# Optimization experiments

Measured on AMD Instinct MI355X. Metric: run time of the kernel, lower is better.

The kernel has to match this reference:

```python
import math
import jax, jax.numpy as jnp
import numpy as np

B, T, D_MODEL, H, D = 2, 1024, 1024, 16, 64
NUM_LEVELS = int(math.ceil(math.log2(T + 1))) + 1  # 12 for max_seq_len=1024


def _fenwick_level(idx):
    return (idx & -idx).bit_length() - 1


def build_fenwick_masks(T, num_levels):
    """NumPy replica of the torch build_fenwick_masks; returns [L, T, T] float32."""
    j_to_nodes = {}
    for j in range(1, T + 1):
        nodes = []
        idx = j
        while idx <= T:
            nodes.append((idx, _fenwick_level(idx)))
            idx += idx & -idx
        j_to_nodes[j] = nodes
    t_to_query_nodes = {}
    for t in range(1, T + 1):
        s = set()
        idx = t
        while idx > 0:
            s.add(idx)
            idx -= idx & -idx
        t_to_query_nodes[t] = s
    masks = np.zeros((num_levels, T, T), dtype=np.float32)
    for t in range(1, T + 1):
        qn = t_to_query_nodes[t]
        for j in range(1, t + 1):
            for node_idx, node_level in j_to_nodes[j]:
                if node_idx in qn:
                    masks[min(node_level, num_levels - 1), t - 1, j - 1] = 1.0
                    break
    return masks


def setup_inputs() -> dict:
    key = jax.random.key(0)
    ks = jax.random.split(key, 8)
    s = 0.02
    return {
        "x": jax.random.normal(ks[0], (B, T, D_MODEL), jnp.float32),
        "qw": jax.random.normal(ks[1], (D_MODEL, H * D), jnp.float32) * s,
        "qb": jnp.zeros((H * D,), jnp.float32),
        "kw": jax.random.normal(ks[2], (D_MODEL, H * D), jnp.float32) * s,
        "kb": jnp.zeros((H * D,), jnp.float32),
        "vw": jax.random.normal(ks[3], (D_MODEL, H * D), jnp.float32) * s,
        "vb": jnp.zeros((H * D,), jnp.float32),
        "lw": jax.random.normal(ks[4], (D_MODEL, H * NUM_LEVELS), jnp.float32) * s,
        "lb": jnp.zeros((H * NUM_LEVELS,), jnp.float32),
        "ow": jax.random.normal(ks[5], (H * D, D_MODEL), jnp.float32) * s,
        "ob": jnp.zeros((D_MODEL,), jnp.float32),
        "level_masks": jnp.asarray(build_fenwick_masks(T, NUM_LEVELS)),
    }


def reference(x, qw, qb, kw, kb, vw, vb, lw, lb, ow, ob, level_masks):
    b, t, _ = x.shape
    phi = lambda a: jax.nn.elu(a) + 1.0  # ELU+1 feature map
    # projections -> [B, H, T, D]
    Q = (x @ qw + qb).reshape(b, t, H, D).transpose(0, 2, 1, 3)
    K = (x @ kw + kb).reshape(b, t, H, D).transpose(0, 2, 1, 3)
    V = (x @ vw + vb).reshape(b, t, H, D).transpose(0, 2, 1, 3)
    Qp, Kp = phi(Q), phi(K)
    # per-level mixing weights: [B, H, T, L]
    logits = (x @ lw + lb).reshape(b, t, H, NUM_LEVELS).transpose(0, 2, 1, 3)
    w = jax.nn.softmax(logits, axis=-1)
    # scores are level-independent in the original; compute once
    S = jnp.einsum('bhid,bhjd->bhij', Qp, Kp)
    # sum_l w_l * mask_l folded into one weighted mask: [B, H, T, T]
    Mw = jnp.einsum('bhil,lij->bhij', w, level_masks)
    Sm = S * Mw
    num = jnp.einsum('bhij,bhjd->bhid', Sm, V)
    den = jnp.maximum(jnp.sum(Sm, axis=-1, keepdims=True), 1e-6)
    out = (num / den).transpose(0, 2, 1, 3).reshape(b, t, H * D)
    return out @ ow + ob
```

## Files before the change

### kernel.cpp

```cpp
#include <hip/hip_runtime.h>
#include <math.h>

typedef __bf16 bf16;
typedef __attribute__((ext_vector_type(4))) __bf16 bf16x4;
typedef __attribute__((ext_vector_type(8))) __bf16 bf16x8;
typedef __attribute__((ext_vector_type(4))) float f32x4;

#define B_SZ 2
#define T_SZ 1024
#define DM_SZ 1024
#define H_SZ 16
#define D_SZ 64
#define L_SZ 12
#define M_ROWS 2048
#define N_PAD 3328

__device__ __forceinline__ f32x4 mfma_16x16x32(bf16x8 a, bf16x8 b, f32x4 c) {
  return __builtin_amdgcn_mfma_f32_16x16x32_bf16(a, b, c, 0, 0, 0);
}

__device__ __forceinline__ void gload_lds16(const bf16* g, bf16* l) {
  __builtin_amdgcn_global_load_lds((const __attribute__((address_space(1))) void*)g,
                                   (__attribute__((address_space(3))) void*)l,
                                   16, 0, 0);
}

__global__ __launch_bounds__(256) void k_prep(
    const float* __restrict__ x, bf16* __restrict__ xb,
    const float* __restrict__ qw, const float* __restrict__ kw,
    const float* __restrict__ vw, const float* __restrict__ ow,
    const float* __restrict__ lw,
    bf16* __restrict__ wqkvT, bf16* __restrict__ owT) {
  const int z = blockIdx.z;
  const int t = threadIdx.x;
  if (z == 5) {
    const size_t base = ((size_t)blockIdx.y * 16 + blockIdx.x) * 8192 + t * 32;
#pragma unroll
    for (int u = 0; u < 4; ++u) {
      const float* p = x + base + u * 8;
      f32x4 a = *(const f32x4*)p;
      f32x4 b = *(const f32x4*)(p + 4);
      bf16x8 o;
#pragma unroll
      for (int e = 0; e < 4; ++e) { o[e] = (bf16)a[e]; o[e + 4] = (bf16)b[e]; }
      *(bf16x8*)(xb + base + u * 8) = o;
    }
    return;
  }
  __shared__ __align__(16) bf16 tile[64][66];
  const float* in; bf16* out; int C = 1024;
  if (z == 0)      { in = qw; out = wqkvT; }
  else if (z == 1) { in = kw; out = wqkvT + (size_t)1024 * DM_SZ; }
  else if (z == 2) { in = vw; out = wqkvT + (size_t)2048 * DM_SZ; }
  else if (z == 3) { in = ow; out = owT; }
  else             { in = lw; out = wqkvT + (size_t)3072 * DM_SZ; C = 192;
                     if (blockIdx.x >= 3) return; }
  const int tc = blockIdx.x * 64;
  const int tr = blockIdx.y * 64;
  const int r = t >> 2;
  const int c4 = (t & 3) << 4;
  const float* src = in + (size_t)(tr + r) * C + tc + c4;
  f32x4 f0 = *(const f32x4*)(src);
  f32x4 f1 = *(const f32x4*)(src + 4);
  f32x4 f2 = *(const f32x4*)(src + 8);
  f32x4 f3 = *(const f32x4*)(src + 12);
#pragma unroll
  for (int e = 0; e < 4; ++e) {
    tile[r][c4 + e]      = (bf16)f0[e];
    tile[r][c4 + 4 + e]  = (bf16)f1[e];
    tile[r][c4 + 8 + e]  = (bf16)f2[e];
    tile[r][c4 + 12 + e] = (bf16)f3[e];
  }
  __syncthreads();
  bf16x8 w0, w1;
#pragma unroll
  for (int e = 0; e < 8; ++e) { w0[e] = tile[c4 + e][r]; w1[e] = tile[c4 + 8 + e][r]; }
  bf16* dst = out + (size_t)(tc + r) * DM_SZ + tr + c4;
  *(bf16x8*)(dst) = w0;
  *(bf16x8*)(dst + 8) = w1;
}

__global__ __launch_bounds__(256) void k_gemm_qkvl(
    const bf16* __restrict__ A, const bf16* __restrict__ Wt,
    const float* __restrict__ qb, const float* __restrict__ kb,
    const float* __restrict__ vb, const float* __restrict__ lb,
    bf16* __restrict__ Qp, bf16* __restrict__ Kp,
    bf16* __restrict__ VTg, float* __restrict__ logit) {
  __shared__ __align__(16) char smem[49152];
  bf16* Asb = (bf16*)smem;
  bf16* Bsb = Asb + 12288;
  const int nb = blockIdx.x * 128;
  const int mb = blockIdx.y * 128;
  const int t = threadIdx.x;
  const int wv = t >> 6;
  const int lane = t & 63;
  const int l16 = lane & 15;
  const int quad = lane >> 4;
  const int wm = (wv & 1) * 64;
  const int wn = (wv >> 1) * 64;

  const int trow = t >> 2;
  const int tcol = (((t & 3) ^ ((t >> 3) & 3)) * 8);
  const int csw = (l16 >> 1) & 3;

  const f32x4 zero4 = {0.f, 0.f, 0.f, 0.f};
  f32x4 acc[4][4];
#pragma unroll
  for (int i = 0; i < 4; ++i)
#pragma unroll
    for (int j = 0; j < 4; ++j) acc[i][j] = zero4;

  const bf16* ag = A + (size_t)(mb + trow) * DM_SZ + tcol;
  const bf16* bg = Wt + (size_t)(nb + trow) * DM_SZ + tcol;

  auto stage = [&](int k0, int buf) {
    bf16* As = Asb + buf * 4096;
    bf16* Bs = Bsb + buf * 4096;
    gload_lds16(ag + k0, As + t * 8);
    gload_lds16(ag + (size_t)64 * DM_SZ + k0, As + 2048 + t * 8);
    gload_lds16(bg + k0, Bs + t * 8);
    gload_lds16(bg + (size_t)64 * DM_SZ + k0, Bs + 2048 + t * 8);
  };

  auto computeStep = [&](int buf) {
    const bf16* As = Asb + buf * 4096;
    const bf16* Bs = Bsb + buf * 4096;
    bf16x8 af[4];
#pragma unroll
    for (int mi = 0; mi < 4; ++mi)
      af[mi] = *(const bf16x8*)(As + (wm + mi * 16 + l16) * 32 + (quad ^ csw) * 8);
#pragma unroll
    for (int ni = 0; ni < 4; ++ni) {
      bf16x8 bfr = *(const bf16x8*)(Bs + (wn + ni * 16 + l16) * 32 + (quad ^ csw) * 8);
#pragma unroll
      for (int mi = 0; mi < 4; ++mi)
        acc[mi][ni] = mfma_16x16x32(af[mi], bfr, acc[mi][ni]);
    }
  };

  stage(0, 0);
  stage(32, 1);
  int cb = 0, sb = 2;
  for (int k0 = 0; k0 < DM_SZ - 32; k0 += 32) {
    asm volatile("s_waitcnt vmcnt(4)" ::: "memory");
    __builtin_amdgcn_s_barrier();
    __builtin_amdgcn_sched_barrier(0);
    if (k0 + 64 < DM_SZ) stage(k0 + 64, sb);
    computeStep(cb);
    cb = (cb == 2) ? 0 : cb + 1;
    sb = (sb == 2) ? 0 : sb + 1;
  }
  asm volatile("s_waitcnt vmcnt(0)" ::: "memory");
  __builtin_amdgcn_s_barrier();
  __builtin_amdgcn_sched_barrier(0);
  computeStep(cb);

  const int seg = nb >> 10;
  if (seg < 2) {
    const float* bias = seg == 0 ? qb : kb;
    bf16* outp = seg == 0 ? Qp : Kp;
    const int c0 = (nb & 1023) + wn;
#pragma unroll
    for (int ni = 0; ni < 4; ++ni) {
      const int col = c0 + ni * 16 + l16;
      const float bv = bias[col];
#pragma unroll
      for (int mi = 0; mi < 4; ++mi) {
#pragma unroll
        for (int r = 0; r < 4; ++r) {
          const int row = mb + wm + mi * 16 + quad * 4 + r;
          float v = acc[mi][ni][r] + bv;
          v = (v > 0.f) ? (v + 1.f) : __expf(v);
          outp[(size_t)row * DM_SZ + col] = (bf16)v;
        }
      }
    }
  } else if (seg == 2) {
    bf16* Trt = (bf16*)smem;
    const int cb2 = nb - 2048;
    __syncthreads();
#pragma unroll
    for (int ni = 0; ni < 4; ++ni) {
      const int nloc = wn + ni * 16 + l16;
      const float bv = vb[cb2 + nloc];
#pragma unroll
      for (int mi = 0; mi < 4; ++mi) {
        const int mloc = wm + mi * 16 + quad * 4;
        bf16x4 pk;
#pragma unroll
        for (int r = 0; r < 4; ++r) pk[r] = (bf16)(acc[mi][ni][r] + bv);
        *(bf16x4*)&Trt[nloc * 136 + mloc] = pk;
      }
    }
    __syncthreads();
    const int dn = t >> 1, ch = t & 1;
    const int bq = mb >> 10;
    const int m0g = mb & 1023;
    bf16* dst = VTg + ((size_t)(bq * 1024 + cb2 + dn)) * T_SZ + m0g + ch * 64;
    const bf16* srcl = Trt + dn * 136 + ch * 64;
#pragma unroll
    for (int e = 0; e < 8; ++e)
      *(bf16x8*)(dst + e * 8) = *(const bf16x8*)(srcl + e * 8);
  } else {
    const int lc0 = (nb - 3072) + wn;
#pragma unroll
    for (int ni = 0; ni < 4; ++ni) {
      const int lcol = lc0 + ni * 16 + l16;
      if (lcol < H_SZ * L_SZ) {
        const float bv = lb[lcol];
#pragma unroll
        for (int mi = 0; mi < 4; ++mi) {
#pragma unroll
          for (int r = 0; r < 4; ++r) {
            const int row = mb + wm + mi * 16 + quad * 4 + r;
            logit[(size_t)row * (H_SZ * L_SZ) + lcol] = acc[mi][ni][r] + bv;
          }
        }
      }
    }
  }
}

__global__ __launch_bounds__(256) void k_build(const bf16* __restrict__ Kp,
                                               const bf16* __restrict__ VTg,
                                               float* __restrict__ Hbuf,
                                               float* __restrict__ ksumbuf) {
  __shared__ __align__(16) bf16 KTs[64][72];
  __shared__ __align__(16) bf16 VTs[64][72];
  const int idx = blockIdx.x;
  const int bh = idx & 31;
  const int jt = idx >> 5;
  const int b = bh >> 4, h = bh & 15;
  const int t = threadIdx.x;
  const int wv = t >> 6, lane = t & 63, l16 = lane & 15, quad = lane >> 4;
  const int r = t >> 2, c = (t & 3) << 4;

  const bf16* vp = VTg + ((size_t)bh * 64 + r) * T_SZ + jt * 64 + c;
  bf16x8 v0 = *(const bf16x8*)vp;
  bf16x8 v1 = *(const bf16x8*)(vp + 8);
  const bf16* kp = Kp + ((size_t)b * T_SZ + jt * 64 + r) * DM_SZ + h * 64 + c;
  bf16x8 k0 = *(const bf16x8*)kp;
  bf16x8 k1 = *(const bf16x8*)(kp + 8);
  *(bf16x8*)&VTs[r][c] = v0;
  *(bf16x8*)&VTs[r][c + 8] = v1;
#pragma unroll
  for (int e = 0; e < 8; ++e) { KTs[c + e][r] = k0[e]; KTs[c + 8 + e][r] = k1[e]; }
  __syncthreads();

  if (t < 64) {
    float s = 0.f;
#pragma unroll
    for (int j = 0; j < 64; ++j) s += (float)KTs[t][j];
    ksumbuf[((size_t)bh * 16 + jt) * 64 + t] = s;
  }

  const f32x4 zero4 = {0.f, 0.f, 0.f, 0.f};
  f32x4 acc[4];
#pragma unroll
  for (int tn = 0; tn < 4; ++tn) acc[tn] = zero4;
#pragma unroll
  for (int ks = 0; ks < 2; ++ks) {
    bf16x8 af = *(const bf16x8*)&VTs[wv * 16 + l16][ks * 32 + quad * 8];
#pragma unroll
    for (int tn = 0; tn < 4; ++tn) {
      bf16x8 bfr = *(const bf16x8*)&KTs[tn * 16 + l16][ks * 32 + quad * 8];
      acc[tn] = mfma_16x16x32(af, bfr, acc[tn]);
    }
  }
  float* hp = Hbuf + ((size_t)bh * 16 + jt) * 4096;
#pragma unroll
  for (int tn = 0; tn < 4; ++tn)
#pragma unroll
    for (int rr = 0; rr < 4; ++rr)
      hp[(wv * 16 + quad * 4 + rr) * 64 + tn * 16 + l16] = acc[tn][rr];
}

__global__ __launch_bounds__(256) void k_attn(const bf16* __restrict__ Qp,
                                              const bf16* __restrict__ Kp,
                                              const bf16* __restrict__ VTg,
                                              const float* __restrict__ Lg,
                                              const float* __restrict__ Hbuf,
                                              const float* __restrict__ ksumbuf,
                                              bf16* __restrict__ O) {
  __shared__ __align__(16) bf16 Ks[64][72];
  __shared__ __align__(16) bf16 VTs[64][72];
  __shared__ __align__(16) bf16 Ms[4][64][72];
  __shared__ __align__(16) bf16 Pl[4][16][80];
  __shared__ __align__(16) bf16 Bdvs[16][72];
  __shared__ float Ws[64 * L_SZ];
  __shared__ float q63s[64];
  __shared__ float y63s[64];
  __shared__ float dsum63s;

  const int idx = blockIdx.x;
  const int s = idx >> 5;
  const int bh = idx & 31;
  const int it = (s < 8) ? (15 - s) : (s - 8);
  const int b = bh >> 4;
  const int h = bh & 15;
  const int i0 = it * 64;
  const int t = threadIdx.x;
  const int wv = t >> 6;
  const int lane = t & 63;
  const int l16 = lane & 15;
  const int quad = lane >> 4;
  const int m0 = wv * 16;
  const size_t base_bt = (size_t)b * T_SZ;

  for (int i = t; i < 16 * 72; i += 256) ((short*)Bdvs)[i] = 0;
  if (t < 64) y63s[t] = 0.f;
  if (t == 0) dsum63s = 0.f;

  const bf16* qptr = Qp + (base_bt + i0 + m0 + l16) * DM_SZ + h * 64 + quad * 8;
  const bf16x8 aq0 = *(const bf16x8*)(qptr);
  const bf16x8 aq1 = *(const bf16x8*)(qptr + 32);

  if (t < 64) q63s[t] = (float)Qp[(base_bt + i0 + 63) * DM_SZ + h * 64 + t];

  const int sr = t >> 2;
  const int sc = (t & 3) << 4;
  const bf16* kpg = Kp + (base_bt + i0 + sr) * DM_SZ + h * 64 + sc;
  const bf16x8 kv0 = *(const bf16x8*)(kpg);
  const bf16x8 kv1 = *(const bf16x8*)(kpg + 8);
  const bf16* vpg = VTg + ((size_t)bh * 64 + sr) * T_SZ + i0 + sc;
  const bf16x8 vv0 = *(const bf16x8*)(vpg);
  const bf16x8 vv1 = *(const bf16x8*)(vpg + 8);

  if (t < 64) {
    const float* lp = Lg + (base_bt + i0 + t) * (H_SZ * L_SZ) + h * L_SZ;
    float v[L_SZ];
    float m = -1e30f;
#pragma unroll
    for (int l = 0; l < L_SZ; ++l) { v[l] = lp[l]; m = fmaxf(m, v[l]); }
    float sum = 0.f;
#pragma unroll
    for (int l = 0; l < L_SZ; ++l) { v[l] = __expf(v[l] - m); sum += v[l]; }
    const float inv = 1.f / sum;
#pragma unroll
    for (int l = 0; l < L_SZ; ++l) Ws[t * L_SZ + l] = v[l] * inv;
  }

  __syncthreads();

  *(bf16x8*)&Ks[sr][sc] = kv0;
  *(bf16x8*)&Ks[sr][sc + 8] = kv1;
  *(bf16x8*)&VTs[sr][sc] = vv0;
  *(bf16x8*)&VTs[sr][sc + 8] = vv1;

  const int il_base = m0 + quad * 4;
  const f32x4 zero4 = {0.f, 0.f, 0.f, 0.f};
  f32x4 accn[4];
#pragma unroll
  for (int tn = 0; tn < 4; ++tn) accn[tn] = zero4;
  float den[4] = {0.f, 0.f, 0.f, 0.f};

  if (it > 0) {
    const float* hb = Hbuf + (size_t)bh * 16 * 4096;
    const float* ksb = ksumbuf + (size_t)bh * 16 * 64;
    f32x4 m63a[4];
#pragma unroll
    for (int i = 0; i < 4; ++i) m63a[i] = zero4;
    float dv63 = 0.f;
    int x = it;
    while (x > 0) {
      const int g = __builtin_ctz((unsigned)x);
      const int lo = x - (1 << g);
      f32x4 ma[4];
#pragma unroll
      for (int i = 0; i < 4; ++i) ma[i] = zero4;
      float dva = 0.f;
      for (int jt = lo; jt < x; ++jt) {
        const float wB = Ws[63 * L_SZ + 6 + (31 - __clz((unsigned)((it + 1) ^ jt)))];
        const float* lp = hb + jt * 4096 + t * 16;
#pragma unroll
        for (int i = 0; i < 4; ++i) {
          f32x4 hv = *(const f32x4*)(lp + i * 4);
#pragma unroll
          for (int e = 0; e < 4; ++e) {
            ma[i][e] += hv[e];
            m63a[i][e] += wB * hv[e];
          }
        }
        if (t < 64) {
          const float ksv = ksb[jt * 64 + t];
          dva += ksv;
          dv63 += wB * ksv;
        }
      }
      bf16x8 o0, o1;
#pragma unroll
      for (int e = 0; e < 4; ++e) {
        o0[e] = (bf16)ma[0][e]; o0[e + 4] = (bf16)ma[1][e];
        o1[e] = (bf16)ma[2][e]; o1[e + 4] = (bf16)ma[3][e];
      }
      *(bf16x8*)&Ms[g][t >> 2][(t & 3) << 4] = o0;
      *(bf16x8*)&Ms[g][t >> 2][((t & 3) << 4) + 8] = o1;
      if (t < 64) Bdvs[g][t] = (bf16)dva;
      x = lo;
    }
    float p63 = 0.f;
    const int d1b = (t & 3) << 4;
#pragma unroll
    for (int i = 0; i < 4; ++i)
#pragma unroll
      for (int e = 0; e < 4; ++e) p63 += q63s[d1b + i * 4 + e] * m63a[i][e];
    p63 += __shfl_xor(p63, 1, 64);
    p63 += __shfl_xor(p63, 2, 64);
    if ((t & 3) == 0) y63s[t >> 2] = p63;
    if (t < 64) {
      float pd = q63s[t] * dv63;
      pd += __shfl_xor(pd, 1, 64);
      pd += __shfl_xor(pd, 2, 64);
      pd += __shfl_xor(pd, 4, 64);
      pd += __shfl_xor(pd, 8, 64);
      pd += __shfl_xor(pd, 16, 64);
      pd += __shfl_xor(pd, 32, 64);
      if (t == 0) dsum63s = pd;
    }
  }
  __syncthreads();

  if (it > 0) {
    int x = it;
    while (x > 0) {
      const int g = __builtin_ctz((unsigned)x);
      f32x4 ya[4];
#pragma unroll
      for (int tn = 0; tn < 4; ++tn) ya[tn] = zero4;
#pragma unroll
      for (int ks = 0; ks < 2; ++ks) {
        const bf16x8 af = ks ? aq1 : aq0;
#pragma unroll
        for (int tn = 0; tn < 4; ++tn) {
          bf16x8 bfr = *(const bf16x8*)&Ms[g][tn * 16 + l16][ks * 32 + quad * 8];
          ya[tn] = mfma_16x16x32(af, bfr, ya[tn]);
        }
      }
      float wg[4];
#pragma unroll
      for (int r = 0; r < 4; ++r) {
        const int il = il_base + r;
        wg[r] = (il == 63) ? 0.f : Ws[il * L_SZ + 6 + g];
      }
#pragma unroll
      for (int tn = 0; tn < 4; ++tn)
#pragma unroll
        for (int r = 0; r < 4; ++r) accn[tn][r] += wg[r] * ya[tn][r];
      x -= 1 << g;
    }
    f32x4 da = zero4;
#pragma unroll
    for (int ks = 0; ks < 2; ++ks) {
      const bf16x8 af = ks ? aq1 : aq0;
      bf16x8 bfr = *(const bf16x8*)&Bdvs[l16][ks * 32 + quad * 8];
      da = mfma_16x16x32(af, bfr, da);
    }
#pragma unroll
    for (int r = 0; r < 4; ++r) {
      const int il = il_base + r;
      const float wd = (il == 63) ? 0.f : Ws[il * L_SZ + 6 + (l16 & 3)];
      den[r] += wd * da[r];
    }
  }

  {
    f32x4 sacc[4];
    __builtin_amdgcn_s_setprio(1);
#pragma unroll
    for (int tn = 0; tn < 4; ++tn) {
      sacc[tn] = zero4;
      bf16x8 bk0 = *(const bf16x8*)&Ks[tn * 16 + l16][quad * 8];
      bf16x8 bk1 = *(const bf16x8*)&Ks[tn * 16 + l16][32 + quad * 8];
      sacc[tn] = mfma_16x16x32(aq0, bk0, sacc[tn]);
      sacc[tn] = mfma_16x16x32(aq1, bk1, sacc[tn]);
    }
    __builtin_amdgcn_s_setprio(0);
#pragma unroll
    for (int tn = 0; tn < 4; ++tn) {
#pragma unroll
      for (int r = 0; r < 4; ++r) {
        const int il = il_base + r;
        const int ig = i0 + il;
        const int jg = i0 + tn * 16 + l16;
        float p = 0.f;
        if (jg <= ig) {
          const int lvl = 31 - __clz((unsigned)((ig + 1) ^ jg));
          p = sacc[tn][r] * Ws[il * L_SZ + lvl];
        }
        den[r] += p;
        Pl[wv][quad * 4 + r][(tn * 16 + l16) ^ (quad << 4)] = (bf16)p;
      }
    }
    __builtin_amdgcn_s_setprio(1);
#pragma unroll
    for (int ks = 0; ks < 2; ++ks) {
      bf16x8 apf = *(const bf16x8*)&Pl[wv][l16][(ks * 32 + quad * 8) ^ ((l16 >> 2) << 4)];
#pragma unroll
      for (int tn = 0; tn < 4; ++tn) {
        bf16x8 bvf = *(const bf16x8*)&VTs[tn * 16 + l16][ks * 32 + quad * 8];
        accn[tn] = mfma_16x16x32(apf, bvf, accn[tn]);
      }
    }
    __builtin_amdgcn_s_setprio(0);
  }

#pragma unroll
  for (int r = 0; r < 4; ++r) {
    float d = den[r];
    d += __shfl_xor(d, 1, 64);
    d += __shfl_xor(d, 2, 64);
    d += __shfl_xor(d, 4, 64);
    d += __shfl_xor(d, 8, 64);
    den[r] = d;
  }
  if (il_base + 3 == 63) den[3] += dsum63s;
#pragma unroll
  for (int r = 0; r < 4; ++r) den[r] = fmaxf(den[r], 1e-6f);

#pragma unroll
  for (int tn = 0; tn < 4; ++tn) {
#pragma unroll
    for (int r = 0; r < 4; ++r) {
      const int il = il_base + r;
      float v = accn[tn][r];
      if (il == 63) v += y63s[tn * 16 + l16];
      O[(base_bt + i0 + il) * DM_SZ + h * 64 + tn * 16 + l16] =
          (bf16)(v / den[r]);
    }
  }
}

__global__ __launch_bounds__(256) void k_gemm_out(const bf16* __restrict__ A,
                                                  const bf16* __restrict__ Wt,
                                                  const float* __restrict__ ob,
                                                  float* __restrict__ out) {
  __shared__ __align__(16) bf16 As[3][2048];
  __shared__ __align__(16) bf16 Bs[3][2048];
  const int nb = blockIdx.x * 64;
  const int mb = blockIdx.y * 64;
  const int t = threadIdx.x;
  const int wv = t >> 6;
  const int lane = t & 63;
  const int l16 = lane & 15;
  const int quad = lane >> 4;
  const int wm = wv * 16;

  const int trow = t >> 2;
  const int tcol = (((t & 3) ^ ((t >> 3) & 3)) * 8);
  const int csw = (l16 >> 1) & 3;

  const f32x4 zero4 = {0.f, 0.f, 0.f, 0.f};
  f32x4 acc[4];
#pragma unroll
  for (int j = 0; j < 4; ++j) acc[j] = zero4;

  const bf16* ag = A + (size_t)(mb + trow) * DM_SZ + tcol;
  const bf16* bg = Wt + (size_t)(nb + trow) * DM_SZ + tcol;

  auto stageg = [&](int k0, int buf) {
    gload_lds16(ag + k0, As[buf] + t * 8);
    gload_lds16(bg + k0, Bs[buf] + t * 8);
  };
  auto computeStep = [&](int buf) {
    bf16x8 af = *(const bf16x8*)(As[buf] + (wm + l16) * 32 + (quad ^ csw) * 8);
#pragma unroll
    for (int ni = 0; ni < 4; ++ni) {
      bf16x8 bfr = *(const bf16x8*)(Bs[buf] + (ni * 16 + l16) * 32 + (quad ^ csw) * 8);
      acc[ni] = mfma_16x16x32(af, bfr, acc[ni]);
    }
  };

  stageg(0, 0);
  stageg(32, 1);
  int cb = 0, sb = 2;
  for (int k0 = 0; k0 < DM_SZ - 32; k0 += 32) {
    asm volatile("s_waitcnt vmcnt(2)" ::: "memory");
    __builtin_amdgcn_s_barrier();
    __builtin_amdgcn_sched_barrier(0);
    if (k0 + 64 < DM_SZ) stageg(k0 + 64, sb);
    computeStep(cb);
    cb = (cb == 2) ? 0 : cb + 1;
    sb = (sb == 2) ? 0 : sb + 1;
  }
  asm volatile("s_waitcnt vmcnt(0)" ::: "memory");
  __builtin_amdgcn_s_barrier();
  __builtin_amdgcn_sched_barrier(0);
  computeStep(cb);

#pragma unroll
  for (int ni = 0; ni < 4; ++ni) {
    const int col = nb + ni * 16 + l16;
    const float bv = ob[col];
#pragma unroll
    for (int r = 0; r < 4; ++r) {
      const int row = mb + wm + quad * 4 + r;
      out[(size_t)row * DM_SZ + col] = acc[ni][r] + bv;
    }
  }
}

extern "C" void kernel_launch(void* const* d_in, const int* in_sizes, int n_in,
                              void* d_out, int out_size, void* d_ws, size_t ws_size,
                              hipStream_t stream) {
  (void)in_sizes; (void)n_in; (void)out_size; (void)ws_size;
  const float* x  = (const float*)d_in[0];
  const float* qw = (const float*)d_in[1];
  const float* qb = (const float*)d_in[2];
  const float* kw = (const float*)d_in[3];
  const float* kb = (const float*)d_in[4];
  const float* vw = (const float*)d_in[5];
  const float* vb = (const float*)d_in[6];
  const float* lw = (const float*)d_in[7];
  const float* lb = (const float*)d_in[8];
  const float* ow = (const float*)d_in[9];
  const float* ob = (const float*)d_in[10];

  char* ws = (char*)d_ws;
  size_t off = 0;
  auto alloc = [&](size_t bytes) -> char* {
    char* p = ws + off;
    off += (bytes + 255) & ~(size_t)255;
    return p;
  };
  bf16* xb     = (bf16*)alloc((size_t)M_ROWS * DM_SZ * 2);
  bf16* wqkvT  = (bf16*)alloc((size_t)N_PAD * DM_SZ * 2);
  bf16* owT    = (bf16*)alloc((size_t)DM_SZ * DM_SZ * 2);
  bf16* Qp     = (bf16*)alloc((size_t)M_ROWS * DM_SZ * 2);
  bf16* Kpb    = (bf16*)alloc((size_t)M_ROWS * DM_SZ * 2);
  bf16* VTg    = (bf16*)alloc((size_t)M_ROWS * DM_SZ * 2);
  bf16* attn   = (bf16*)alloc((size_t)M_ROWS * DM_SZ * 2);
  float* logit = (float*)alloc((size_t)M_ROWS * H_SZ * L_SZ * 4);
  float* Hbuf  = (float*)alloc((size_t)32 * 16 * 4096 * 4);
  float* ksumb = (float*)alloc((size_t)32 * 16 * 64 * 4);

  const dim3 blk(256);
  k_prep<<<dim3(16, 16, 6), blk, 0, stream>>>(x, xb, qw, kw, vw, ow, lw, wqkvT, owT);
  k_gemm_qkvl<<<dim3(N_PAD / 128, M_ROWS / 128), blk, 0, stream>>>(
      xb, wqkvT, qb, kb, vb, lb, Qp, Kpb, VTg, logit);
  k_build<<<dim3(32 * 16), blk, 0, stream>>>(Kpb, VTg, Hbuf, ksumb);
  k_attn<<<dim3((T_SZ / 64) * B_SZ * H_SZ), blk, 0, stream>>>(
      Qp, Kpb, VTg, logit, Hbuf, ksumb, attn);
  k_gemm_out<<<dim3(DM_SZ / 64, M_ROWS / 64), blk, 0, stream>>>(attn, owT, ob, (float*)d_out);
}
```

Baseline: 172.2 us.

## Load QKVL GEMM B operand directly into registers, bypassing LDS

The fused QKV/level projection GEMM now reads the weight (B) fragments straight from global memory into registers, triple-buffered across k-steps, and only stages the A tile through LDS. This shrinks shared memory use and removes the LDS round trip and ds_read traffic for B, which may allow higher occupancy. It also drops the XOR swizzle on the A tile, which can bring back LDS bank conflicts. The per-lane global B loads are less coalesced, each wave fetches B separately, and the register pressure from three B fragment sets is higher.

```diff
diff --git a/kernel.cpp b/kernel.cpp
--- a/kernel.cpp
+++ b/kernel.cpp
@@ -86,9 +86,8 @@
     const float* __restrict__ vb, const float* __restrict__ lb,
     bf16* __restrict__ Qp, bf16* __restrict__ Kp,
     bf16* __restrict__ VTg, float* __restrict__ logit) {
-  __shared__ __align__(16) char smem[49152];
+  __shared__ __align__(16) char smem[34816];
   bf16* Asb = (bf16*)smem;
-  bf16* Bsb = Asb + 12288;
   const int nb = blockIdx.x * 128;
   const int mb = blockIdx.y * 128;
   const int t = threadIdx.x;
@@ -100,8 +99,7 @@
   const int wn = (wv >> 1) * 64;
 
   const int trow = t >> 2;
-  const int tcol = (((t & 3) ^ ((t >> 3) & 3)) * 8);
-  const int csw = (l16 >> 1) & 3;
+  const int tcol = (t & 3) * 8;
 
   const f32x4 zero4 = {0.f, 0.f, 0.f, 0.f};
   f32x4 acc[4][4];
@@ -111,49 +109,67 @@
     for (int j = 0; j < 4; ++j) acc[i][j] = zero4;
 
   const bf16* ag = A + (size_t)(mb + trow) * DM_SZ + tcol;
-  const bf16* bg = Wt + (size_t)(nb + trow) * DM_SZ + tcol;
-
-  auto stage = [&](int k0, int buf) {
+  const bf16* bp0 = Wt + (size_t)(nb + wn + 0 * 16 + l16) * DM_SZ + quad * 8;
+  const bf16* bp1 = Wt + (size_t)(nb + wn + 1 * 16 + l16) * DM_SZ + quad * 8;
+  const bf16* bp2 = Wt + (size_t)(nb + wn + 2 * 16 + l16) * DM_SZ + quad * 8;
+  const bf16* bp3 = Wt + (size_t)(nb + wn + 3 * 16 + l16) * DM_SZ + quad * 8;
+
+  bf16x8 B0[4], B1[4], B2[4];
+
+  auto stageA = [&](int k0, int buf) {
     bf16* As = Asb + buf * 4096;
-    bf16* Bs = Bsb + buf * 4096;
     gload_lds16(ag + k0, As + t * 8);
     gload_lds16(ag + (size_t)64 * DM_SZ + k0, As + 2048 + t * 8);
-    gload_lds16(bg + k0, Bs + t * 8);
-    gload_lds16(bg + (size_t)64 * DM_SZ + k0, Bs + 2048 + t * 8);
   };
 
-  auto computeStep = [&](int buf) {
-    const bf16* As = Asb + buf * 4096;
-    const bf16* Bs = Bsb + buf * 4096;
-    bf16x8 af[4];
-#pragma unroll
-    for (int mi = 0; mi < 4; ++mi)
-      af[mi] = *(const bf16x8*)(As + (wm + mi * 16 + l16) * 32 + (quad ^ csw) * 8);
-#pragma unroll
-    for (int ni = 0; ni < 4; ++ni) {
-      bf16x8 bfr = *(const bf16x8*)(Bs + (wn + ni * 16 + l16) * 32 + (quad ^ csw) * 8);
-#pragma unroll
-      for (int mi = 0; mi < 4; ++mi)
-        acc[mi][ni] = mfma_16x16x32(af[mi], bfr, acc[mi][ni]);
-    }
-  };
-
-  stage(0, 0);
-  stage(32, 1);
-  int cb = 0, sb = 2;
-  for (int k0 = 0; k0 < DM_SZ - 32; k0 += 32) {
-    asm volatile("s_waitcnt vmcnt(4)" ::: "memory");
-    __builtin_amdgcn_s_barrier();
-    __builtin_amdgcn_sched_barrier(0);
-    if (k0 + 64 < DM_SZ) stage(k0 + 64, sb);
-    computeStep(cb);
-    cb = (cb == 2) ? 0 : cb + 1;
-    sb = (sb == 2) ? 0 : sb + 1;
-  }
-  asm volatile("s_waitcnt vmcnt(0)" ::: "memory");
-  __builtin_amdgcn_s_barrier();
+#define LOADB(SET, K0)                                   \
+  {                                                      \
+    SET[0] = *(const bf16x8*)(bp0 + (K0));               \
+    SET[1] = *(const bf16x8*)(bp1 + (K0));               \
+    SET[2] = *(const bf16x8*)(bp2 + (K0));               \
+    SET[3] = *(const bf16x8*)(bp3 + (K0));               \
+  }
+
+#define QCOMPUTE(BUF, SET)                                                   \
+  {                                                                          \
+    const bf16* As_ = Asb + (BUF) * 4096;                                    \
+    bf16x8 af[4];                                                            \
+    _Pragma("unroll") for (int mi = 0; mi < 4; ++mi)                         \
+        af[mi] = *(const bf16x8*)(As_ + (wm + mi * 16 + l16) * 32 + quad * 8); \
+    _Pragma("unroll") for (int ni = 0; ni < 4; ++ni)                         \
+        _Pragma("unroll") for (int mi = 0; mi < 4; ++mi)                     \
+            acc[mi][ni] = mfma_16x16x32(af[mi], SET[ni], acc[mi][ni]);       \
+  }
+
+#define QWAIT(VM)                                        \
+  asm volatile("s_waitcnt vmcnt(" #VM ")" ::: "memory"); \
+  __builtin_amdgcn_s_barrier();                          \
   __builtin_amdgcn_sched_barrier(0);
-  computeStep(cb);
+
+  stageA(0, 0);  LOADB(B0, 0);
+  stageA(32, 1); LOADB(B1, 32);
+
+  int k0 = 0;
+#pragma unroll 1
+  for (int it3 = 0; it3 < 10; ++it3, k0 += 96) {
+    QWAIT(6);
+    stageA(k0 + 64, 2); LOADB(B2, k0 + 64);
+    QCOMPUTE(0, B0);
+    QWAIT(6);
+    stageA(k0 + 96, 0); LOADB(B0, k0 + 96);
+    QCOMPUTE(1, B1);
+    QWAIT(6);
+    stageA(k0 + 128, 1); LOADB(B1, k0 + 128);
+    QCOMPUTE(2, B2);
+  }
+  QWAIT(6);
+  QCOMPUTE(0, B0);
+  QWAIT(0);
+  QCOMPUTE(1, B1);
+
+#undef LOADB
+#undef QCOMPUTE
+#undef QWAIT
 
   const int seg = nb >> 10;
   if (seg < 2) {
```

Result: slower. 189.1 us (+9.8%).
